# Optimization experiments

Measured on AMD Instinct MI355X. Metric: run time of the kernel, lower is better.

Reference implementation:

```python
import jax, jax.numpy as jnp
import numpy as np

D_NUM, P_NUM, LAYER, EMB = 1500, 4500, 3, 128


def _xavier(k, shape):
    lim = float(np.sqrt(6.0 / (shape[0] + shape[1])))
    return jax.random.uniform(k, shape, minval=-lim, maxval=lim, dtype=jnp.float32)


def _sym_norm(adj):
    # D^{-1/2} A D^{-1/2}, zero-degree safe (utils._create_*_adj_mat)
    deg = adj.sum(axis=1)
    dinv = jnp.where(deg > 0, jax.lax.rsqrt(jnp.maximum(deg, 1e-12)), 0.0)
    return adj * dinv[:, None] * dinv[None, :]


def _gcn(adj, emb, num):
    # LightGCN-style propagation: mean of layer-0..num embeddings (utils._gcn)
    def step(e, _):
        e = adj @ e
        return e, e
    _, layers = jax.lax.scan(step, emb, None, length=num)
    return (emb + layers.sum(axis=0)) / (num + 1)


def _neighbor_mean(mat, feats):
    # vectorized form of the per-row python loop: mean of feats over j where mat[i,j]==1, zeros if no neighbor
    m = (mat == 1.0).astype(feats.dtype)
    cnt = m.sum(axis=1, keepdims=True)
    return jnp.where(cnt > 0, (m @ feats) / jnp.maximum(cnt, 1.0), 0.0)


def _get_weight(emb, WA, BA, HA):
    return jax.nn.log_softmax(jax.nn.relu(emb @ WA + BA) @ HA, axis=0)


def setup_inputs():
    k = jax.random.split(jax.random.key(0), 24)
    N = D_NUM + P_NUM
    A = (jax.random.uniform(k[0], (5, N, N)) < 0.005).astype(jnp.float32)
    z = lambda: jnp.zeros((EMB,), jnp.float32)
    h = lambda: jnp.full((EMB, 1), 0.01, jnp.float32)
    return {
        "A": A,
        "drug_structure": jax.random.normal(k[1], (D_NUM, 160), jnp.float32),
        "protein_structure": jax.random.normal(k[2], (P_NUM, 512), jnp.float32),
        "lin_drug_w": _xavier(k[3], (160, EMB)), "lin_drug_b": z(),
        "lin_pro_w": _xavier(k[4], (512, EMB)), "lin_pro_b": z(),
        "p_weight": _xavier(k[5], (EMB, EMB)),
        "d_weight_i": _xavier(k[6], (EMB, EMB)),
        "pd_weight_p": _xavier(k[7], (EMB, EMB)),
        "pd_weight_d": _xavier(k[8], (EMB, EMB)),
        "dp_weight_p": _xavier(k[9], (EMB, EMB)),
        "WA_drug": _xavier(k[10], (EMB, EMB)), "BA_drug": z(), "HA_drug": h(),
        "WB_drug": _xavier(k[11], (EMB, EMB)), "BB_drug": z(), "HB_drug": h(),
        "WA_pro": _xavier(k[12], (EMB, EMB)), "BA_pro": z(), "HA_pro": h(),
        "WB_pro": _xavier(k[13], (EMB, EMB)), "BB_pro": z(), "HB_pro": h(),
        "WA_sim": _xavier(k[14], (EMB, EMB)), "BA_sim": z(), "HA_sim": h(),
        "layer": LAYER,
    }


def reference(A, drug_structure, protein_structure, lin_drug_w, lin_drug_b, lin_pro_w, lin_pro_b,
              p_weight, d_weight_i, pd_weight_p, pd_weight_d, dp_weight_p,
              WA_drug, BA_drug, HA_drug, WB_drug, BB_drug, HB_drug,
              WA_pro, BA_pro, HA_pro, WB_pro, BB_pro, HB_pro,
              WA_sim, BA_sim, HA_sim, layer):
    D, P = D_NUM, P_NUM
    R = A[0, :D, D:D + P]                       # drug-protein relation [D,P]
    dru_str = drug_structure @ lin_drug_w + lin_drug_b      # [D,128]
    pro_str = protein_structure @ lin_pro_w + lin_pro_b     # [P,128]

    def rel_emb(mat, feats, w):
        nei = _neighbor_mean(mat, feats)
        adj = _sym_norm((mat == 1.0).astype(feats.dtype))
        return _gcn(adj, feats @ w, layer), nei

    dru_rel_emb, dru_rel_nei = rel_emb(A[2, :D, :D], dru_str, d_weight_i)
    pro_rel_emb, pro_rel_nei = rel_emb(A[3, D:, D:], pro_str, p_weight)
    dru_sim_emb, dru_sim_nei = rel_emb(A[4, :D, :D], dru_str, d_weight_i)

    dru_tem = _neighbor_mean(R, pro_rel_nei)    # [D,128]
    # NB: torch 'dru_rel_nei + dru_sim_nei' concatenates python LISTS, and only
    # indices < D are ever read, so pro_tem effectively uses dru_rel_nei only.
    pro_tem = _neighbor_mean(R.T, dru_rel_nei)  # [P,128]

    # bipartite symmetric-normalized adjacency [[0,R],[R^T,0]]
    bip = jnp.zeros((D + P, D + P), R.dtype)
    bip = bip.at[:D, D:].set(R).at[D:, :D].set(R.T)
    adj = _sym_norm(bip)

    one_all = 0.8 * dru_str + 0.2 * dru_tem
    two_all = 0.8 * pro_str + 0.2 * pro_tem
    one_emb = dru_str @ pd_weight_d
    two_all = (two_all @ dp_weight_p) @ pd_weight_d
    two_emb = pro_str @ pd_weight_p
    dru_int = _gcn(adj, jnp.concatenate([one_emb, two_all], axis=0), layer)[:D]
    pro_int = _gcn(adj, jnp.concatenate([one_all, two_emb], axis=0), layer)[D:]

    drug_w = _get_weight(dru_int, WA_drug, BA_drug, HA_drug)
    pro_w = _get_weight(pro_int, WA_pro, BA_pro, HA_pro)
    dru_rel_w = _get_weight(dru_rel_emb, WB_drug, BB_drug, HB_drug)
    pro_rel_w = _get_weight(pro_rel_emb, WB_pro, BB_pro, HB_pro)
    dru_sim_w = _get_weight(dru_sim_emb, WA_sim, BA_sim, HA_sim)

    # faithful to source (including its asymmetric renormalization); dropout is eval-mode identity
    a_w = drug_w / (drug_w + dru_rel_w + dru_sim_w)
    b_w = dru_rel_w / (a_w + dru_rel_w + dru_sim_w)
    c_w = 1.0 - a_w - b_w
    fin_dru = a_w * dru_int + b_w * dru_rel_emb + c_w * dru_sim_emb

    pa = pro_w / (pro_w + pro_rel_w)
    pb = 1.0 - pa
    fin_pro = pa * pro_int + pb * pro_rel_emb

    y = fin_dru @ fin_pro.T                     # [D,P]
    y = (y - y.mean()) / jnp.std(y, ddof=1)     # torch.std is unbiased
    return jax.nn.sigmoid(y)
```

## Files before the change

### kernel.cpp

```cpp
#include <hip/hip_runtime.h>

constexpr int CAP = 128;
constexpr int RS_INV = 1, RS_RSQRT = 2, CS_RSQRT = 4, FINALIZE = 8;

struct BuildSeg {
    const float* M; long ldm; int rows; int cols; int col_off;
    int* idx; int* cnt;
};

__global__ void k_build_all(BuildSeg sa, BuildSeg sb, BuildSeg sc, BuildSeg sd,
                            int zb, int e0, int e1, int e2,
                            int* __restrict__ zcnt, int nz, double* __restrict__ stats)
{
    int blk = blockIdx.x;
    if (blk < zb) {
        int i = blk * 256 + threadIdx.x;
        if (i < nz) zcnt[i] = 0;
        if (blk == 0 && threadIdx.x < 2) stats[threadIdx.x] = 0.0;
        return;
    }
    BuildSeg s; int lb;
    if (blk < e0)      { s = sa; lb = blk - zb; }
    else if (blk < e1) { s = sb; lb = blk - e0; }
    else if (blk < e2) { s = sc; lb = blk - e1; }
    else               { s = sd; lb = blk - e2; }
    int row = lb * 4 + (threadIdx.x >> 6);
    if (row >= s.rows) return;
    int lane = threadIdx.x & 63;
    const float* p = s.M + (long)row * s.ldm;
    int* ri = s.idx + (long)row * CAP;
    int base = 0;
    for (int j0 = 0; j0 < s.cols; j0 += 64) {
        int j = j0 + lane;
        bool hit = (j < s.cols) && (p[j] == 1.0f);
        unsigned long long m = __ballot(hit);
        if (hit) {
            int pos = base + (int)__popcll(m & ((1ULL << lane) - 1ULL));
            if (pos < CAP) ri[pos] = j + s.col_off;
        }
        base += (int)__popcll(m);
    }
    if (lane == 0) s.cnt[row] = base < CAP ? base : CAP;
}

__global__ void k_scatter_T(int* __restrict__ idx, int* __restrict__ cnt, int topRows)
{
    int row = blockIdx.x * 4 + (threadIdx.x >> 6);
    if (row >= topRows) return;
    int lane = threadIdx.x & 63;
    int n = cnt[row];
    const int* ri = idx + (long)row * CAP;
    for (int k = lane; k < n; k += 64) {
        int j = ri[k];
        int pos = atomicAdd(&cnt[j], 1);
        if (pos < CAP) idx[(long)j * CAP + pos] = row;
    }
}

struct SpmmJob {
    const int* idx; const int* cnt; int rows; int mod;
    const float* X; float* out; float* acc; const float* init; float* fin;
    int flags;
};

__global__ __launch_bounds__(256)
void k_spmm_multi(SpmmJob ja, SpmmJob jb, int nb0)
{
    SpmmJob j; int lb;
    if ((int)blockIdx.x < nb0) { j = ja; lb = blockIdx.x; }
    else                       { j = jb; lb = blockIdx.x - nb0; }
    int c = threadIdx.x & 127;
    int row = lb * 2 + (threadIdx.x >> 7);
    if (row >= j.rows) return;
    int r_loc = row, xoff = 0;
    if (row >= j.mod) { r_loc = row - j.mod; xoff = j.mod; }
    int n = j.cnt[r_loc];
    const int* ri = j.idx + (long)r_loc * CAP;
    const bool csq = (j.flags & CS_RSQRT) != 0;
    float acc = 0.0f;
    int k = 0;
    for (; k + 4 <= n; k += 4) {
        int c0 = ri[k], c1 = ri[k + 1], c2 = ri[k + 2], c3 = ri[k + 3];
        float x0 = j.X[(long)(c0 + xoff) * 128 + c];
        float x1 = j.X[(long)(c1 + xoff) * 128 + c];
        float x2 = j.X[(long)(c2 + xoff) * 128 + c];
        float x3 = j.X[(long)(c3 + xoff) * 128 + c];
        if (csq) {
            int n0 = j.cnt[c0], n1 = j.cnt[c1], n2 = j.cnt[c2], n3 = j.cnt[c3];
            x0 *= (n0 > 0) ? rsqrtf((float)n0) : 0.0f;
            x1 *= (n1 > 0) ? rsqrtf((float)n1) : 0.0f;
            x2 *= (n2 > 0) ? rsqrtf((float)n2) : 0.0f;
            x3 *= (n3 > 0) ? rsqrtf((float)n3) : 0.0f;
        }
        acc += (x0 + x1) + (x2 + x3);
    }
    for (; k < n; ++k) {
        int cj = ri[k];
        float x = j.X[(long)(cj + xoff) * 128 + c];
        if (csq) {
            int nj = j.cnt[cj];
            x *= (nj > 0) ? rsqrtf((float)nj) : 0.0f;
        }
        acc += x;
    }
    float v;
    if (j.flags & RS_INV)        v = (n > 0) ? acc / (float)n : 0.0f;
    else if (j.flags & RS_RSQRT) v = (n > 0) ? acc * rsqrtf((float)n) : 0.0f;
    else                         v = acc;
    long o = (long)row * 128 + c;
    if (j.flags & FINALIZE) {
        j.fin[o] = (j.acc[o] + v) * 0.25f;
    } else {
        j.out[o] = v;
        if (j.acc) j.acc[o] = (j.init ? j.init[o] : j.acc[o]) + v;
    }
}

struct LinJob {
    const float* X; const float* X2; float pa, pb; int rows; int K;
    const float* W; const float* bias; float* out; float* out2;
};

__global__ __launch_bounds__(256)
void k_lin_multi(LinJob j0, LinJob j1, LinJob j2, LinJob j3,
                 int e0, int e1, int e2)
{
    __shared__ float Ws[64 * 128];
    LinJob j; int lb;
    int blk = blockIdx.x;
    if (blk < e0)      { j = j0; lb = blk; }
    else if (blk < e1) { j = j1; lb = blk - e0; }
    else if (blk < e2) { j = j2; lb = blk - e1; }
    else               { j = j3; lb = blk - e2; }
    int c = threadIdx.x & 127;
    int row = lb * 2 + (threadIdx.x >> 7);
    if (j.W == nullptr) {
        if (row < j.rows) {
            long o = (long)row * 128 + c;
            float v = j.pa * j.X[o] + j.pb * j.X2[o];
            j.out[o] = v;
            if (j.out2) j.out2[o] = v;
        }
        return;
    }
    float acc = 0.0f;
    for (int k0 = 0; k0 < j.K; k0 += 64) {
        int chunk = min(64, j.K - k0);
        for (int e = threadIdx.x; e < chunk * 128; e += 256)
            Ws[e] = j.W[(long)(k0 + (e >> 7)) * 128 + (e & 127)];
        __syncthreads();
        if (row < j.rows) {
            const float* xr = j.X + (long)row * j.K + k0;
            const float* x2r = j.X2 ? j.X2 + (long)row * j.K + k0 : nullptr;
            #pragma unroll 4
            for (int kk = 0; kk < chunk; ++kk) {
                float v = xr[kk];
                if (j.X2) v = j.pa * v + j.pb * x2r[kk];
                acc += v * Ws[kk * 128 + c];
            }
        }
        __syncthreads();
    }
    if (row < j.rows) {
        float v = acc + (j.bias ? j.bias[c] : 0.0f);
        j.out[(long)row * 128 + c] = v;
        if (j.out2) j.out2[(long)row * 128 + c] = v;
    }
}

struct AttnJob { const float* X; int rows; const float* W; const float* B;
                 const float* H; float* s; };

__global__ __launch_bounds__(256)
void k_attn_multi(AttnJob a0, AttnJob a1, AttnJob a2, AttnJob a3, AttnJob a4,
                  int e0, int e1, int e2, int e3)
{
    __shared__ float Ws[64 * 128];
    __shared__ float part[4];
    AttnJob j; int lb;
    int blk = blockIdx.x;
    if (blk < e0)      { j = a0; lb = blk; }
    else if (blk < e1) { j = a1; lb = blk - e0; }
    else if (blk < e2) { j = a2; lb = blk - e1; }
    else if (blk < e3) { j = a3; lb = blk - e2; }
    else               { j = a4; lb = blk - e3; }
    int c = threadIdx.x & 127;
    int row = lb * 2 + (threadIdx.x >> 7);
    float acc = 0.0f;
    for (int k0 = 0; k0 < 128; k0 += 64) {
        for (int e = threadIdx.x; e < 64 * 128; e += 256)
            Ws[e] = j.W[(long)(k0 + (e >> 7)) * 128 + (e & 127)];
        __syncthreads();
        if (row < j.rows) {
            const float* xr = j.X + (long)row * 128 + k0;
            #pragma unroll 4
            for (int kk = 0; kk < 64; ++kk)
                acc += xr[kk] * Ws[kk * 128 + c];
        }
        __syncthreads();
    }
    float v = 0.0f;
    if (row < j.rows) v = fmaxf(acc + j.B[c], 0.0f) * j.H[c];
    for (int o = 32; o > 0; o >>= 1) v += __shfl_down(v, o, 64);
    if ((threadIdx.x & 63) == 0) part[threadIdx.x >> 6] = v;
    __syncthreads();
    if (threadIdx.x == 0 && row < j.rows)   j.s[row] = part[0] + part[1];
    if (threadIdx.x == 128 && row < j.rows) j.s[row] = part[2] + part[3];
}

__global__ void k_logsoftmax5(float* s0, int n0, float* s1, int n1,
                              float* s2, int n2, float* s3, int n3,
                              float* s4, int n4)
{
    float* s; int n;
    switch (blockIdx.x) {
        case 0: s = s0; n = n0; break;
        case 1: s = s1; n = n1; break;
        case 2: s = s2; n = n2; break;
        case 3: s = s3; n = n3; break;
        default: s = s4; n = n4; break;
    }
    __shared__ float red[256];
    int t = threadIdx.x;
    float m = -3.4e38f;
    for (int i = t; i < n; i += 256) m = fmaxf(m, s[i]);
    red[t] = m; __syncthreads();
    for (int o = 128; o > 0; o >>= 1) {
        if (t < o) red[t] = fmaxf(red[t], red[t + o]);
        __syncthreads();
    }
    m = red[0];
    __syncthreads();
    float sum = 0.0f;
    for (int i = t; i < n; i += 256) sum += expf(s[i] - m);
    red[t] = sum; __syncthreads();
    for (int o = 128; o > 0; o >>= 1) {
        if (t < o) red[t] += red[t + o];
        __syncthreads();
    }
    float lse = m + logf(red[0]);
    for (int i = t; i < n; i += 256) s[i] -= lse;
}

__global__ void k_fin(const float* __restrict__ wd, const float* __restrict__ wdr,
                      const float* __restrict__ wds,
                      const float* __restrict__ ei, const float* __restrict__ er,
                      const float* __restrict__ es,
                      const float* __restrict__ wp, const float* __restrict__ wpr,
                      const float* __restrict__ pi, const float* __restrict__ pr,
                      float* __restrict__ fd, float* __restrict__ fp,
                      long nDel, long total)
{
    long i = (long)blockIdx.x * 256 + threadIdx.x;
    if (i >= total) return;
    if (i < nDel) {
        int r = (int)(i >> 7);
        float aL = wd[r], bL = wdr[r], cL = wds[r];
        float a = aL / (aL + bL + cL);
        float b = bL / (a + bL + cL);
        float c = 1.0f - a - b;
        fd[i] = a * ei[i] + b * er[i] + c * es[i];
    } else {
        long k = i - nDel;
        int r = (int)(k >> 7);
        float pa = wp[r] / (wp[r] + wpr[r]);
        fp[k] = pa * pi[k] + (1.0f - pa) * pr[k];
    }
}

__global__ __launch_bounds__(256)
void k_ygemm(const float* __restrict__ Af, const float* __restrict__ Bf,
             int M, int N, float* __restrict__ y, double* __restrict__ stats)
{
    __shared__ float Ast[32][68];
    __shared__ float Bst[32][68];
    int i0 = blockIdx.y * 64, j0 = blockIdx.x * 64;
    int tx = threadIdx.x & 15, ty = threadIdx.x >> 4;
    float acc[4][4] = {};
    for (int k0 = 0; k0 < 128; k0 += 32) {
        for (int e = threadIdx.x; e < 64 * 32; e += 256) {
            int r = e >> 5, kk = e & 31;
            int ia = i0 + r, jb = j0 + r;
            Ast[kk][r] = (ia < M) ? Af[(long)ia * 128 + k0 + kk] : 0.0f;
            Bst[kk][r] = (jb < N) ? Bf[(long)jb * 128 + k0 + kk] : 0.0f;
        }
        __syncthreads();
        #pragma unroll 8
        for (int kk = 0; kk < 32; ++kk) {
            float a0 = Ast[kk][ty * 4 + 0], a1 = Ast[kk][ty * 4 + 1];
            float a2 = Ast[kk][ty * 4 + 2], a3 = Ast[kk][ty * 4 + 3];
            float b0 = Bst[kk][tx * 4 + 0], b1 = Bst[kk][tx * 4 + 1];
            float b2 = Bst[kk][tx * 4 + 2], b3 = Bst[kk][tx * 4 + 3];
            acc[0][0] += a0 * b0; acc[0][1] += a0 * b1; acc[0][2] += a0 * b2; acc[0][3] += a0 * b3;
            acc[1][0] += a1 * b0; acc[1][1] += a1 * b1; acc[1][2] += a1 * b2; acc[1][3] += a1 * b3;
            acc[2][0] += a2 * b0; acc[2][1] += a2 * b1; acc[2][2] += a2 * b2; acc[2][3] += a2 * b3;
            acc[3][0] += a3 * b0; acc[3][1] += a3 * b1; acc[3][2] += a3 * b2; acc[3][3] += a3 * b3;
        }
        __syncthreads();
    }
    double s1 = 0.0, s2 = 0.0;
    #pragma unroll
    for (int q = 0; q < 4; ++q) {
        int i = i0 + ty * 4 + q;
        if (i < M) {
            #pragma unroll
            for (int p = 0; p < 4; ++p) {
                int j = j0 + tx * 4 + p;
                if (j < N) {
                    float v = acc[q][p];
                    y[(long)i * N + j] = v;
                    s1 += v; s2 += (double)v * v;
                }
            }
        }
    }
    __shared__ double r1[256];
    __shared__ double r2[256];
    r1[threadIdx.x] = s1; r2[threadIdx.x] = s2;
    __syncthreads();
    for (int o = 128; o > 0; o >>= 1) {
        if (threadIdx.x < o) {
            r1[threadIdx.x] += r1[threadIdx.x + o];
            r2[threadIdx.x] += r2[threadIdx.x + o];
        }
        __syncthreads();
    }
    if (threadIdx.x == 0) {
        atomicAdd(&stats[0], r1[0]);
        atomicAdd(&stats[1], r2[0]);
    }
}

__global__ void k_sigmoid(const float* __restrict__ y, const double* __restrict__ stats,
                          long n, float* __restrict__ out)
{
    long i = (long)blockIdx.x * 256 + threadIdx.x;
    if (i >= n) return;
    double nd = (double)n;
    double mean = stats[0] / nd;
    double var = (stats[1] - nd * mean * mean) / (nd - 1.0);
    if (var < 1e-30) var = 1e-30;
    float inv = (float)(1.0 / sqrt(var));
    float mu = (float)mean;
    out[i] = 1.0f / (1.0f + expf(-((y[i] - mu) * inv)));
}

extern "C" void kernel_launch(void* const* d_in, const int* in_sizes, int n_in,
                              void* d_out, int out_size, void* d_ws, size_t ws_size,
                              hipStream_t stream)
{
    constexpr int D = 1500, P = 4500, E = 128;
    constexpr int NB = D + P;
    constexpr int NR = D + P + D;
    constexpr long ALD = 6000;
    constexpr long ASZ = 36000000L;

    const float* A    = (const float*)d_in[0];
    const float* drug_structure    = (const float*)d_in[1];
    const float* protein_structure = (const float*)d_in[2];
    const float* lin_drug_w = (const float*)d_in[3];
    const float* lin_drug_b = (const float*)d_in[4];
    const float* lin_pro_w  = (const float*)d_in[5];
    const float* lin_pro_b  = (const float*)d_in[6];
    const float* p_weight   = (const float*)d_in[7];
    const float* d_weight_i = (const float*)d_in[8];
    const float* pd_weight_p = (const float*)d_in[9];
    const float* pd_weight_d = (const float*)d_in[10];
    const float* dp_weight_p = (const float*)d_in[11];
    const float* WA_drug = (const float*)d_in[12];
    const float* BA_drug = (const float*)d_in[13];
    const float* HA_drug = (const float*)d_in[14];
    const float* WB_drug = (const float*)d_in[15];
    const float* BB_drug = (const float*)d_in[16];
    const float* HB_drug = (const float*)d_in[17];
    const float* WA_pro = (const float*)d_in[18];
    const float* BA_pro = (const float*)d_in[19];
    const float* HA_pro = (const float*)d_in[20];
    const float* WB_pro = (const float*)d_in[21];
    const float* BB_pro = (const float*)d_in[22];
    const float* HB_pro = (const float*)d_in[23];
    const float* WA_sim = (const float*)d_in[24];
    const float* BA_sim = (const float*)d_in[25];
    const float* HA_sim = (const float*)d_in[26];

    const float* Rp  = A + 1500;
    const float* A2p = A + 2 * ASZ;
    const float* A3p = A + 3 * ASZ + 1500 * ALD + 1500;
    const float* A4p = A + 4 * ASZ;

    char* wsbase = (char*)d_ws;
    size_t off = 0;
    auto alloc = [&](size_t bytes) -> void* {
        off = (off + 255) & ~(size_t)255;
        void* p = wsbase + off;
        off += bytes;
        return p;
    };
    int*   idx_bip  = (int*)alloc((size_t)NB * CAP * 4);
    int*   cnt_bip  = (int*)alloc((size_t)NB * 4);
    int*   idx_rel  = (int*)alloc((size_t)NR * CAP * 4);
    int*   cnt_rel  = (int*)alloc((size_t)NR * 4);
    float* str_s    = (float*)alloc((size_t)NR * E * 4);
    float* nei_s    = (float*)alloc((size_t)NR * E * 4);
    float* cur_s    = (float*)alloc((size_t)NR * E * 4);
    float* nxt_s    = (float*)alloc((size_t)NR * E * 4);
    float* acc_s    = (float*)alloc((size_t)NR * E * 4);
    float* emb_s    = (float*)alloc((size_t)NR * E * 4);
    float* tem_s    = (float*)alloc((size_t)NB * E * 4);
    float* big_cur  = (float*)alloc((size_t)2 * NB * E * 4);
    float* big_nxt  = (float*)alloc((size_t)2 * NB * E * 4);
    float* big_acc  = (float*)alloc((size_t)2 * NB * E * 4);
    float* int_s    = (float*)alloc((size_t)2 * NB * E * 4);
    float* W2       = (float*)alloc((size_t)E * E * 4);
    float* w_drug = (float*)alloc(D * 4);
    float* w_drel = (float*)alloc(D * 4);
    float* w_dsim = (float*)alloc(D * 4);
    float* w_pro  = (float*)alloc(P * 4);
    float* w_prel = (float*)alloc(P * 4);
    float* fin_dru = (float*)alloc((size_t)D * E * 4);
    float* fin_pro = (float*)alloc((size_t)P * E * 4);
    float* ybuf    = (float*)alloc((size_t)D * P * 4);
    double* stats  = (double*)alloc(2 * sizeof(double));
    (void)ws_size; (void)in_sizes; (void)n_in; (void)out_size;

    float* dru_str = str_s;
    float* pro_str = str_s + (size_t)D * E;
    float* dru_rel_emb = emb_s;
    float* pro_rel_emb = emb_s + (size_t)D * E;
    float* dru_sim_emb = emb_s + (size_t)NB * E;
    float* dru_tem = tem_s;
    float* pro_tem = tem_s + (size_t)D * E;
    float* dru_int = int_s;
    float* pro_int = int_s + (size_t)(NB + D) * E;

    long nD = (long)D * E, nP = (long)P * E;

    SpmmJob JZ = {};
    LinJob  LZ = {};

    {
        BuildSeg sR  = { Rp,  ALD, D, P, D,  idx_bip, cnt_bip };
        BuildSeg sA2 = { A2p, ALD, D, D, 0,  idx_rel, cnt_rel };
        BuildSeg sA3 = { A3p, ALD, P, P, D,  idx_rel + (size_t)D * CAP,  cnt_rel + D };
        BuildSeg sA4 = { A4p, ALD, D, D, NB, idx_rel + (size_t)NB * CAP, cnt_rel + NB };
        int zb = (P + 255) / 256;
        int e0 = zb + (D + 3) / 4;
        int e1 = e0 + (D + 3) / 4;
        int e2 = e1 + (P + 3) / 4;
        int total = e2 + (D + 3) / 4;
        k_build_all<<<total, 256, 0, stream>>>(sR, sA2, sA3, sA4, zb, e0, e1, e2,
                                               cnt_bip + D, P, stats);
    }
    k_scatter_T<<<(D + 3) / 4, 256, 0, stream>>>(idx_bip, cnt_bip, D);

    {
        LinJob jd = { drug_structure, nullptr, 0, 0, D, 160, lin_drug_w, lin_drug_b,
                      dru_str, str_s + (size_t)NB * E };
        LinJob jp = { protein_structure, nullptr, 0, 0, P, 512, lin_pro_w, lin_pro_b,
                      pro_str, nullptr };
        LinJob jw = { dp_weight_p, nullptr, 0, 0, E, E, pd_weight_d, nullptr, W2, nullptr };
        int e0 = (D + 1) / 2, e1 = e0 + (P + 1) / 2, e2 = e1 + (E + 1) / 2;
        k_lin_multi<<<e2, 256, 0, stream>>>(jd, jp, jw, LZ, e0, e1, e2);
    }
    {
        SpmmJob jn = { idx_rel, cnt_rel, NR, NR, str_s, nei_s, nullptr, nullptr, nullptr, RS_INV };
        k_spmm_multi<<<(NR + 1) / 2, 256, 0, stream>>>(jn, JZ, (NR + 1) / 2);
    }
    {
        LinJob jd = { dru_str, nullptr, 0, 0, D, E, d_weight_i, nullptr,
                      cur_s, cur_s + (size_t)NB * E };
        LinJob jp = { pro_str, nullptr, 0, 0, P, E, p_weight, nullptr,
                      cur_s + (size_t)D * E, nullptr };
        int e0 = (D + 1) / 2, e1 = e0 + (P + 1) / 2;
        k_lin_multi<<<e1, 256, 0, stream>>>(jd, jp, LZ, LZ, e0, e1, e1);
    }
    {
        SpmmJob j1 = { idx_rel, cnt_rel, NR, NR, cur_s, nxt_s, acc_s, cur_s, nullptr,
                       RS_RSQRT | CS_RSQRT };
        SpmmJob j2 = { idx_bip, cnt_bip, NB, NB, nei_s, tem_s, nullptr, nullptr, nullptr,
                       RS_INV };
        int nb0 = (NR + 1) / 2, nb1 = (NB + 1) / 2;
        k_spmm_multi<<<nb0 + nb1, 256, 0, stream>>>(j1, j2, nb0);
    }
    {
        LinJob j0 = { dru_str, nullptr, 0, 0, D, E, pd_weight_d, nullptr, big_cur, nullptr };
        LinJob j1 = { pro_str, pro_tem, 0.8f, 0.2f, P, E, W2, nullptr, big_cur + nD, nullptr };
        LinJob j2 = { dru_str, dru_tem, 0.8f, 0.2f, D, E, nullptr, nullptr,
                      big_cur + (size_t)NB * E, nullptr };
        LinJob j3 = { pro_str, nullptr, 0, 0, P, E, pd_weight_p, nullptr,
                      big_cur + (size_t)(NB + D) * E, nullptr };
        int e0 = (D + 1) / 2, e1 = e0 + (P + 1) / 2, e2 = e1 + (D + 1) / 2;
        int tt = e2 + (P + 1) / 2;
        k_lin_multi<<<tt, 256, 0, stream>>>(j0, j1, j2, j3, e0, e1, e2);
    }
    {
        SpmmJob j1 = { idx_rel, cnt_rel, NR, NR, nxt_s, cur_s, acc_s, nullptr, nullptr,
                       RS_RSQRT | CS_RSQRT };
        SpmmJob j2 = { idx_bip, cnt_bip, 2 * NB, NB, big_cur, big_nxt, big_acc, big_cur,
                       nullptr, RS_RSQRT | CS_RSQRT };
        int nb0 = (NR + 1) / 2;
        k_spmm_multi<<<nb0 + NB, 256, 0, stream>>>(j1, j2, nb0);
    }
    {
        SpmmJob j1 = { idx_rel, cnt_rel, NR, NR, cur_s, nullptr, acc_s, nullptr, emb_s,
                       RS_RSQRT | CS_RSQRT | FINALIZE };
        SpmmJob j2 = { idx_bip, cnt_bip, 2 * NB, NB, big_nxt, big_cur, big_acc, nullptr,
                       nullptr, RS_RSQRT | CS_RSQRT };
        int nb0 = (NR + 1) / 2;
        k_spmm_multi<<<nb0 + NB, 256, 0, stream>>>(j1, j2, nb0);
    }
    {
        SpmmJob j2 = { idx_bip, cnt_bip, 2 * NB, NB, big_cur, nullptr, big_acc, nullptr,
                       int_s, RS_RSQRT | CS_RSQRT | FINALIZE };
        k_spmm_multi<<<NB, 256, 0, stream>>>(j2, JZ, NB);
    }
    {
        AttnJob a0 = { dru_int,     D, WA_drug, BA_drug, HA_drug, w_drug };
        AttnJob a1 = { pro_int,     P, WA_pro,  BA_pro,  HA_pro,  w_pro  };
        AttnJob a2 = { dru_rel_emb, D, WB_drug, BB_drug, HB_drug, w_drel };
        AttnJob a3 = { pro_rel_emb, P, WB_pro,  BB_pro,  HB_pro,  w_prel };
        AttnJob a4 = { dru_sim_emb, D, WA_sim,  BA_sim,  HA_sim,  w_dsim };
        int e0 = (D + 1) / 2, e1 = e0 + (P + 1) / 2, e2 = e1 + (D + 1) / 2;
        int e3 = e2 + (P + 1) / 2, tt = e3 + (D + 1) / 2;
        k_attn_multi<<<tt, 256, 0, stream>>>(a0, a1, a2, a3, a4, e0, e1, e2, e3);
    }
    k_logsoftmax5<<<5, 256, 0, stream>>>(w_drug, D, w_pro, P, w_drel, D, w_prel, P, w_dsim, D);

    {
        long total = nD + nP;
        k_fin<<<(int)((total + 255) / 256), 256, 0, stream>>>(
            w_drug, w_drel, w_dsim, dru_int, dru_rel_emb, dru_sim_emb,
            w_pro, w_prel, pro_int, pro_rel_emb,
            fin_dru, fin_pro, nD, total);
    }
    dim3 yg((P + 63) / 64, (D + 63) / 64);
    k_ygemm<<<yg, 256, 0, stream>>>(fin_dru, fin_pro, D, P, ybuf, stats);
    long ny = (long)D * P;
    k_sigmoid<<<(int)((ny + 255) / 256), 256, 0, stream>>>(ybuf, stats, ny, (float*)d_out);
}
```

Before: 1.373 ms.

## Fuse all stages into one cooperative persistent kernel with grid syncs

Replaces the chain of separate launches (build, scatter, linear, spmm, attention, softmax, fin, gemm, sigmoid) with a single cooperative kernel of 512 persistent blocks that loops over tiles and uses grid-wide syncs between dependent phases. Independent work is placed together in the same phase, such as the relation spmm with linear jobs and the attention on relation embeddings with a bipartite spmm layer. The goal is to remove per-launch overhead and idle gaps between small kernels. In exchange it adds grid-sync cost, caps parallelism at the fixed grid size, hardcodes job tile boundaries for these problem sizes, and the sigmoid now uses float4 with no tail handling.

```diff
diff --git a/kernel.cpp b/kernel.cpp
--- a/kernel.cpp
+++ b/kernel.cpp
@@ -1,29 +1,54 @@
 #include <hip/hip_runtime.h>
+#include <hip/hip_cooperative_groups.h>
+
+namespace cg = cooperative_groups;
 
 constexpr int CAP = 128;
 constexpr int RS_INV = 1, RS_RSQRT = 2, CS_RSQRT = 4, FINALIZE = 8;
-
-struct BuildSeg {
-    const float* M; long ldm; int rows; int cols; int col_off;
-    int* idx; int* cnt;
+constexpr int GRID = 512;
+
+struct BuildSeg { const float* M; long ldm; int rows; int cols; int col_off;
+                  int* idx; int* cnt; };
+struct LinJob  { const float* X; const float* X2; float pa, pb; int rows; int K;
+                 const float* W; const float* bias; float* out; float* out2; };
+struct SpmmJob { const int* idx; const int* cnt; int rows; int mod;
+                 const float* X; float* out; float* acc; const float* init;
+                 float* fin; int flags; };
+struct AttnJob { const float* X; int rows; const float* W; const float* B;
+                 const float* H; float* s; };
+
+struct MegaArgs {
+    BuildSeg bs[4]; int bsEnd[4];
+    int* zcnt; int nz; double* stats;
+    int* idx_bip; int* cnt_bip; int scatterUnits; int scatterTop;
+    LinJob pj[3]; int pjEnd[3];
+    SpmmJob relNei;
+    LinJob rj[2]; int rjEnd[2];
+    SpmmJob relL1, bipNei;
+    LinJob bj[4]; int bjEnd[4];
+    SpmmJob relL2;
+    SpmmJob bipL1, relL3;
+    SpmmJob bipL2;
+    AttnJob atR[3]; int atREnd[3];
+    SpmmJob bipL3;
+    float* smv[5]; int smn[5];
+    AttnJob atI[2]; int atIEnd[2];
+    const float *wd, *wdr, *wds, *ei, *er, *es, *wp, *wpr, *pi, *pr;
+    float *fd, *fp; long nDel, totFin;
+    const float *Af, *Bf; int M, N; float* y;
+    float* outp; long ny;
 };
 
-__global__ void k_build_all(BuildSeg sa, BuildSeg sb, BuildSeg sc, BuildSeg sd,
-                            int zb, int e0, int e1, int e2,
-                            int* __restrict__ zcnt, int nz, double* __restrict__ stats)
-{
-    int blk = blockIdx.x;
-    if (blk < zb) {
-        int i = blk * 256 + threadIdx.x;
-        if (i < nz) zcnt[i] = 0;
-        if (blk == 0 && threadIdx.x < 2) stats[threadIdx.x] = 0.0;
-        return;
-    }
-    BuildSeg s; int lb;
-    if (blk < e0)      { s = sa; lb = blk - zb; }
-    else if (blk < e1) { s = sb; lb = blk - e0; }
-    else if (blk < e2) { s = sc; lb = blk - e1; }
-    else               { s = sd; lb = blk - e2; }
+union SharedU {
+    float Ws[64 * 128];
+    struct { float Ast[32][68]; float Bst[32][68];
+             double r1[256]; double r2[256]; } yg;
+    float red[256];
+};
+
+
+__device__ __forceinline__ void build_unit(const BuildSeg& s, int lb)
+{
     int row = lb * 4 + (threadIdx.x >> 6);
     if (row >= s.rows) return;
     int lane = threadIdx.x & 63;
@@ -31,21 +56,21 @@
     int* ri = s.idx + (long)row * CAP;
     int base = 0;
     for (int j0 = 0; j0 < s.cols; j0 += 64) {
-        int j = j0 + lane;
-        bool hit = (j < s.cols) && (p[j] == 1.0f);
+        int jj = j0 + lane;
+        bool hit = (jj < s.cols) && (p[jj] == 1.0f);
         unsigned long long m = __ballot(hit);
         if (hit) {
             int pos = base + (int)__popcll(m & ((1ULL << lane) - 1ULL));
-            if (pos < CAP) ri[pos] = j + s.col_off;
+            if (pos < CAP) ri[pos] = jj + s.col_off;
         }
         base += (int)__popcll(m);
     }
     if (lane == 0) s.cnt[row] = base < CAP ? base : CAP;
 }
 
-__global__ void k_scatter_T(int* __restrict__ idx, int* __restrict__ cnt, int topRows)
-{
-    int row = blockIdx.x * 4 + (threadIdx.x >> 6);
+__device__ __forceinline__ void scatter_unit(int* idx, int* cnt, int topRows, int lb)
+{
+    int row = lb * 4 + (threadIdx.x >> 6);
     if (row >= topRows) return;
     int lane = threadIdx.x & 63;
     int n = cnt[row];
@@ -57,18 +82,8 @@
     }
 }
 
-struct SpmmJob {
-    const int* idx; const int* cnt; int rows; int mod;
-    const float* X; float* out; float* acc; const float* init; float* fin;
-    int flags;
-};
-
-__global__ __launch_bounds__(256)
-void k_spmm_multi(SpmmJob ja, SpmmJob jb, int nb0)
-{
-    SpmmJob j; int lb;
-    if ((int)blockIdx.x < nb0) { j = ja; lb = blockIdx.x; }
-    else                       { j = jb; lb = blockIdx.x - nb0; }
+__device__ __forceinline__ void spmm_tile(const SpmmJob& j, int lb)
+{
     int c = threadIdx.x & 127;
     int row = lb * 2 + (threadIdx.x >> 7);
     if (row >= j.rows) return;
@@ -116,22 +131,23 @@
     }
 }
 
-struct LinJob {
-    const float* X; const float* X2; float pa, pb; int rows; int K;
-    const float* W; const float* bias; float* out; float* out2;
-};
-
-__global__ __launch_bounds__(256)
-void k_lin_multi(LinJob j0, LinJob j1, LinJob j2, LinJob j3,
-                 int e0, int e1, int e2)
-{
-    __shared__ float Ws[64 * 128];
-    LinJob j; int lb;
-    int blk = blockIdx.x;
-    if (blk < e0)      { j = j0; lb = blk; }
-    else if (blk < e1) { j = j1; lb = blk - e0; }
-    else if (blk < e2) { j = j2; lb = blk - e1; }
-    else               { j = j3; lb = blk - e2; }
+__device__ void run_spmm1(const SpmmJob& a)
+{
+    int ta = (a.rows + 1) / 2;
+    for (int t = blockIdx.x; t < ta; t += gridDim.x) spmm_tile(a, t);
+}
+
+__device__ void run_spmm2(const SpmmJob& a, const SpmmJob& b)
+{
+    int ta = (a.rows + 1) / 2, tb = (b.rows + 1) / 2;
+    for (int t = blockIdx.x; t < ta + tb; t += gridDim.x) {
+        if (t < ta) spmm_tile(a, t);
+        else        spmm_tile(b, t - ta);
+    }
+}
+
+__device__ void lin_tile(const LinJob& j, int lb, float* Ws)
+{
     int c = threadIdx.x & 127;
     int row = lb * 2 + (threadIdx.x >> 7);
     if (j.W == nullptr) {
@@ -168,22 +184,20 @@
     }
 }
 
-struct AttnJob { const float* X; int rows; const float* W; const float* B;
-                 const float* H; float* s; };
-
-__global__ __launch_bounds__(256)
-void k_attn_multi(AttnJob a0, AttnJob a1, AttnJob a2, AttnJob a3, AttnJob a4,
-                  int e0, int e1, int e2, int e3)
-{
-    __shared__ float Ws[64 * 128];
+__device__ void run_lin(const LinJob* jobs, const int* ends, int nj, float* Ws)
+{
+    int tot = ends[nj - 1];
+    for (int t = blockIdx.x; t < tot; t += gridDim.x) {
+        int ji = 0;
+        while (t >= ends[ji]) ++ji;
+        int lb = t - (ji ? ends[ji - 1] : 0);
+        lin_tile(jobs[ji], lb, Ws);
+    }
+}
+
+__device__ void attn_tile(const AttnJob& j, int lb, float* Ws)
+{
     __shared__ float part[4];
-    AttnJob j; int lb;
-    int blk = blockIdx.x;
-    if (blk < e0)      { j = a0; lb = blk; }
-    else if (blk < e1) { j = a1; lb = blk - e0; }
-    else if (blk < e2) { j = a2; lb = blk - e1; }
-    else if (blk < e3) { j = a3; lb = blk - e2; }
-    else               { j = a4; lb = blk - e3; }
     int c = threadIdx.x & 127;
     int row = lb * 2 + (threadIdx.x >> 7);
     float acc = 0.0f;
@@ -208,19 +222,19 @@
     if (threadIdx.x == 128 && row < j.rows) j.s[row] = part[2] + part[3];
 }
 
-__global__ void k_logsoftmax5(float* s0, int n0, float* s1, int n1,
-                              float* s2, int n2, float* s3, int n3,
-                              float* s4, int n4)
-{
-    float* s; int n;
-    switch (blockIdx.x) {
-        case 0: s = s0; n = n0; break;
-        case 1: s = s1; n = n1; break;
-        case 2: s = s2; n = n2; break;
-        case 3: s = s3; n = n3; break;
-        default: s = s4; n = n4; break;
-    }
-    __shared__ float red[256];
+__device__ void run_attn(const AttnJob* jobs, const int* ends, int nj, float* Ws)
+{
+    int tot = ends[nj - 1];
+    for (int t = blockIdx.x; t < tot; t += gridDim.x) {
+        int ji = 0;
+        while (t >= ends[ji]) ++ji;
+        int lb = t - (ji ? ends[ji - 1] : 0);
+        attn_tile(jobs[ji], lb, Ws);
+    }
+}
+
+__device__ void softmax_vec(float* s, int n, float* red)
+{
     int t = threadIdx.x;
     float m = -3.4e38f;
     for (int i = t; i < n; i += 256) m = fmaxf(m, s[i]);
@@ -242,55 +256,46 @@
     for (int i = t; i < n; i += 256) s[i] -= lse;
 }
 
-__global__ void k_fin(const float* __restrict__ wd, const float* __restrict__ wdr,
-                      const float* __restrict__ wds,
-                      const float* __restrict__ ei, const float* __restrict__ er,
-                      const float* __restrict__ es,
-                      const float* __restrict__ wp, const float* __restrict__ wpr,
-                      const float* __restrict__ pi, const float* __restrict__ pr,
-                      float* __restrict__ fd, float* __restrict__ fp,
-                      long nDel, long total)
-{
-    long i = (long)blockIdx.x * 256 + threadIdx.x;
-    if (i >= total) return;
-    if (i < nDel) {
-        int r = (int)(i >> 7);
-        float aL = wd[r], bL = wdr[r], cL = wds[r];
-        float a = aL / (aL + bL + cL);
-        float b = bL / (a + bL + cL);
-        float c = 1.0f - a - b;
-        fd[i] = a * ei[i] + b * er[i] + c * es[i];
-    } else {
-        long k = i - nDel;
-        int r = (int)(k >> 7);
-        float pa = wp[r] / (wp[r] + wpr[r]);
-        fp[k] = pa * pi[k] + (1.0f - pa) * pr[k];
-    }
-}
-
-__global__ __launch_bounds__(256)
-void k_ygemm(const float* __restrict__ Af, const float* __restrict__ Bf,
-             int M, int N, float* __restrict__ y, double* __restrict__ stats)
-{
-    __shared__ float Ast[32][68];
-    __shared__ float Bst[32][68];
-    int i0 = blockIdx.y * 64, j0 = blockIdx.x * 64;
+__device__ void run_fin(const MegaArgs& a)
+{
+    long g = (long)blockIdx.x * 256 + threadIdx.x;
+    long gs = (long)gridDim.x * 256;
+    for (long i = g; i < a.totFin; i += gs) {
+        if (i < a.nDel) {
+            int r = (int)(i >> 7);
+            float aL = a.wd[r], bL = a.wdr[r], cL = a.wds[r];
+            float x = aL / (aL + bL + cL);
+            float y = bL / (x + bL + cL);
+            float z = 1.0f - x - y;
+            a.fd[i] = x * a.ei[i] + y * a.er[i] + z * a.es[i];
+        } else {
+            long k = i - a.nDel;
+            int r = (int)(k >> 7);
+            float pa = a.wp[r] / (a.wp[r] + a.wpr[r]);
+            a.fp[k] = pa * a.pi[k] + (1.0f - pa) * a.pr[k];
+        }
+    }
+}
+
+__device__ void ygemm_tile(const MegaArgs& a, int bx, int by, SharedU& sh)
+{
+    int i0 = by * 64, j0 = bx * 64;
     int tx = threadIdx.x & 15, ty = threadIdx.x >> 4;
     float acc[4][4] = {};
     for (int k0 = 0; k0 < 128; k0 += 32) {
         for (int e = threadIdx.x; e < 64 * 32; e += 256) {
             int r = e >> 5, kk = e & 31;
             int ia = i0 + r, jb = j0 + r;
-            Ast[kk][r] = (ia < M) ? Af[(long)ia * 128 + k0 + kk] : 0.0f;
-            Bst[kk][r] = (jb < N) ? Bf[(long)jb * 128 + k0 + kk] : 0.0f;
+            sh.yg.Ast[kk][r] = (ia < a.M) ? a.Af[(long)ia * 128 + k0 + kk] : 0.0f;
+            sh.yg.Bst[kk][r] = (jb < a.N) ? a.Bf[(long)jb * 128 + k0 + kk] : 0.0f;
         }
         __syncthreads();
         #pragma unroll 8
         for (int kk = 0; kk < 32; ++kk) {
-            float a0 = Ast[kk][ty * 4 + 0], a1 = Ast[kk][ty * 4 + 1];
-            float a2 = Ast[kk][ty * 4 + 2], a3 = Ast[kk][ty * 4 + 3];
-            float b0 = Bst[kk][tx * 4 + 0], b1 = Bst[kk][tx * 4 + 1];
-            float b2 = Bst[kk][tx * 4 + 2], b3 = Bst[kk][tx * 4 + 3];
+            float a0 = sh.yg.Ast[kk][ty * 4 + 0], a1 = sh.yg.Ast[kk][ty * 4 + 1];
+            float a2 = sh.yg.Ast[kk][ty * 4 + 2], a3 = sh.yg.Ast[kk][ty * 4 + 3];
+            float b0 = sh.yg.Bst[kk][tx * 4 + 0], b1 = sh.yg.Bst[kk][tx * 4 + 1];
+            float b2 = sh.yg.Bst[kk][tx * 4 + 2], b3 = sh.yg.Bst[kk][tx * 4 + 3];
             acc[0][0] += a0 * b0; acc[0][1] += a0 * b1; acc[0][2] += a0 * b2; acc[0][3] += a0 * b3;
             acc[1][0] += a1 * b0; acc[1][1] += a1 * b1; acc[1][2] += a1 * b2; acc[1][3] += a1 * b3;
             acc[2][0] += a2 * b0; acc[2][1] += a2 * b1; acc[2][2] += a2 * b2; acc[2][3] += a2 * b3;
@@ -302,47 +307,113 @@
     #pragma unroll
     for (int q = 0; q < 4; ++q) {
         int i = i0 + ty * 4 + q;
-        if (i < M) {
+        if (i < a.M) {
             #pragma unroll
             for (int p = 0; p < 4; ++p) {
                 int j = j0 + tx * 4 + p;
-                if (j < N) {
+                if (j < a.N) {
                     float v = acc[q][p];
-                    y[(long)i * N + j] = v;
+                    a.y[(long)i * a.N + j] = v;
                     s1 += v; s2 += (double)v * v;
                 }
             }
         }
     }
-    __shared__ double r1[256];
-    __shared__ double r2[256];
-    r1[threadIdx.x] = s1; r2[threadIdx.x] = s2;
+    sh.yg.r1[threadIdx.x] = s1; sh.yg.r2[threadIdx.x] = s2;
     __syncthreads();
     for (int o = 128; o > 0; o >>= 1) {
         if (threadIdx.x < o) {
-            r1[threadIdx.x] += r1[threadIdx.x + o];
-            r2[threadIdx.x] += r2[threadIdx.x + o];
+            sh.yg.r1[threadIdx.x] += sh.yg.r1[threadIdx.x + o];
+            sh.yg.r2[threadIdx.x] += sh.yg.r2[threadIdx.x + o];
         }
         __syncthreads();
     }
     if (threadIdx.x == 0) {
-        atomicAdd(&stats[0], r1[0]);
-        atomicAdd(&stats[1], r2[0]);
-    }
-}
-
-__global__ void k_sigmoid(const float* __restrict__ y, const double* __restrict__ stats,
-                          long n, float* __restrict__ out)
-{
-    long i = (long)blockIdx.x * 256 + threadIdx.x;
-    if (i >= n) return;
-    double nd = (double)n;
-    double mean = stats[0] / nd;
-    double var = (stats[1] - nd * mean * mean) / (nd - 1.0);
+        atomicAdd(&a.stats[0], sh.yg.r1[0]);
+        atomicAdd(&a.stats[1], sh.yg.r2[0]);
+    }
+}
+
+__device__ void run_ygemm(const MegaArgs& a, SharedU& sh)
+{
+    int tilesX = (a.N + 63) / 64, tilesY = (a.M + 63) / 64;
+    int tot = tilesX * tilesY;
+    for (int t = blockIdx.x; t < tot; t += gridDim.x)
+        ygemm_tile(a, t % tilesX, t / tilesX, sh);
+}
+
+__device__ void run_sigmoid(const MegaArgs& a)
+{
+    double nd = (double)a.ny;
+    double mean = a.stats[0] / nd;
+    double var = (a.stats[1] - nd * mean * mean) / (nd - 1.0);
     if (var < 1e-30) var = 1e-30;
     float inv = (float)(1.0 / sqrt(var));
     float mu = (float)mean;
-    out[i] = 1.0f / (1.0f + expf(-((y[i] - mu) * inv)));
+    long n4 = a.ny >> 2;
+    const float4* y4 = (const float4*)a.y;
+    float4* o4 = (float4*)a.outp;
+    long g = (long)blockIdx.x * 256 + threadIdx.x;
+    long gs = (long)gridDim.x * 256;
+    for (long i = g; i < n4; i += gs) {
+        float4 v = y4[i];
+        v.x = 1.0f / (1.0f + expf(-((v.x - mu) * inv)));
+        v.y = 1.0f / (1.0f + expf(-((v.y - mu) * inv)));
+        v.z = 1.0f / (1.0f + expf(-((v.z - mu) * inv)));
+        v.w = 1.0f / (1.0f + expf(-((v.w - mu) * inv)));
+        o4[i] = v;
+    }
+}
+
+__global__ __launch_bounds__(256, 2)
+void k_mega(MegaArgs a)
+{
+    cg::grid_group grid = cg::this_grid();
+    __shared__ SharedU sh;
+
+    {
+        long g = (long)blockIdx.x * 256 + threadIdx.x;
+        long gs = (long)gridDim.x * 256;
+        for (long i = g; i < a.nz; i += gs) a.zcnt[i] = 0;
+        if (blockIdx.x == 0 && threadIdx.x < 2) a.stats[threadIdx.x] = 0.0;
+        for (int u = blockIdx.x; u < a.bsEnd[3]; u += gridDim.x) {
+            int si = 0;
+            while (u >= a.bsEnd[si]) ++si;
+            int lb = u - (si ? a.bsEnd[si - 1] : 0);
+            build_unit(a.bs[si], lb);
+        }
+        run_lin(a.pj, a.pjEnd, 3, sh.Ws);
+    }
+    grid.sync();
+    {
+        for (int u = blockIdx.x; u < a.scatterUnits; u += gridDim.x)
+            scatter_unit(a.idx_bip, a.cnt_bip, a.scatterTop, u);
+        run_spmm1(a.relNei);
+        run_lin(a.rj, a.rjEnd, 2, sh.Ws);
+    }
+    grid.sync();
+    run_spmm2(a.relL1, a.bipNei);
+    grid.sync();
+    run_lin(a.bj, a.bjEnd, 4, sh.Ws);
+    run_spmm1(a.relL2);
+    grid.sync();
+    run_spmm2(a.bipL1, a.relL3);
+    grid.sync();
+    run_spmm1(a.bipL2);
+    run_attn(a.atR, a.atREnd, 3, sh.Ws);
+    grid.sync();
+    run_spmm1(a.bipL3);
+    if (blockIdx.x < 3) softmax_vec(a.smv[blockIdx.x], a.smn[blockIdx.x], sh.red);
+    grid.sync();
+    run_attn(a.atI, a.atIEnd, 2, sh.Ws);
+    grid.sync();
+    if (blockIdx.x < 2) softmax_vec(a.smv[3 + blockIdx.x], a.smn[3 + blockIdx.x], sh.red);
+    grid.sync();
+    run_fin(a);
+    grid.sync();
+    run_ygemm(a, sh);
+    grid.sync();
+    run_sigmoid(a);
 }
 
 extern "C" void kernel_launch(void* const* d_in, const int* in_sizes, int n_in,
@@ -435,106 +506,80 @@
 
     long nD = (long)D * E, nP = (long)P * E;
 
-    SpmmJob JZ = {};
-    LinJob  LZ = {};
-
-    {
-        BuildSeg sR  = { Rp,  ALD, D, P, D,  idx_bip, cnt_bip };
-        BuildSeg sA2 = { A2p, ALD, D, D, 0,  idx_rel, cnt_rel };
-        BuildSeg sA3 = { A3p, ALD, P, P, D,  idx_rel + (size_t)D * CAP,  cnt_rel + D };
-        BuildSeg sA4 = { A4p, ALD, D, D, NB, idx_rel + (size_t)NB * CAP, cnt_rel + NB };
-        int zb = (P + 255) / 256;
-        int e0 = zb + (D + 3) / 4;
-        int e1 = e0 + (D + 3) / 4;
-        int e2 = e1 + (P + 3) / 4;
-        int total = e2 + (D + 3) / 4;
-        k_build_all<<<total, 256, 0, stream>>>(sR, sA2, sA3, sA4, zb, e0, e1, e2,
-                                               cnt_bip + D, P, stats);
-    }
-    k_scatter_T<<<(D + 3) / 4, 256, 0, stream>>>(idx_bip, cnt_bip, D);
-
-    {
-        LinJob jd = { drug_structure, nullptr, 0, 0, D, 160, lin_drug_w, lin_drug_b,
-                      dru_str, str_s + (size_t)NB * E };
-        LinJob jp = { protein_structure, nullptr, 0, 0, P, 512, lin_pro_w, lin_pro_b,
-                      pro_str, nullptr };
-        LinJob jw = { dp_weight_p, nullptr, 0, 0, E, E, pd_weight_d, nullptr, W2, nullptr };
-        int e0 = (D + 1) / 2, e1 = e0 + (P + 1) / 2, e2 = e1 + (E + 1) / 2;
-        k_lin_multi<<<e2, 256, 0, stream>>>(jd, jp, jw, LZ, e0, e1, e2);
-    }
-    {
-        SpmmJob jn = { idx_rel, cnt_rel, NR, NR, str_s, nei_s, nullptr, nullptr, nullptr, RS_INV };
-        k_spmm_multi<<<(NR + 1) / 2, 256, 0, stream>>>(jn, JZ, (NR + 1) / 2);
-    }
-    {
-        LinJob jd = { dru_str, nullptr, 0, 0, D, E, d_weight_i, nullptr,
-                      cur_s, cur_s + (size_t)NB * E };
-        LinJob jp = { pro_str, nullptr, 0, 0, P, E, p_weight, nullptr,
-                      cur_s + (size_t)D * E, nullptr };
-        int e0 = (D + 1) / 2, e1 = e0 + (P + 1) / 2;
-        k_lin_multi<<<e1, 256, 0, stream>>>(jd, jp, LZ, LZ, e0, e1, e1);
-    }
-    {
-        SpmmJob j1 = { idx_rel, cnt_rel, NR, NR, cur_s, nxt_s, acc_s, cur_s, nullptr,
-                       RS_RSQRT | CS_RSQRT };
-        SpmmJob j2 = { idx_bip, cnt_bip, NB, NB, nei_s, tem_s, nullptr, nullptr, nullptr,
-                       RS_INV };
-        int nb0 = (NR + 1) / 2, nb1 = (NB + 1) / 2;
-        k_spmm_multi<<<nb0 + nb1, 256, 0, stream>>>(j1, j2, nb0);
-    }
-    {
-        LinJob j0 = { dru_str, nullptr, 0, 0, D, E, pd_weight_d, nullptr, big_cur, nullptr };
-        LinJob j1 = { pro_str, pro_tem, 0.8f, 0.2f, P, E, W2, nullptr, big_cur + nD, nullptr };
-        LinJob j2 = { dru_str, dru_tem, 0.8f, 0.2f, D, E, nullptr, nullptr,
-                      big_cur + (size_t)NB * E, nullptr };
-        LinJob j3 = { pro_str, nullptr, 0, 0, P, E, pd_weight_p, nullptr,
-                      big_cur + (size_t)(NB + D) * E, nullptr };
-        int e0 = (D + 1) / 2, e1 = e0 + (P + 1) / 2, e2 = e1 + (D + 1) / 2;
-        int tt = e2 + (P + 1) / 2;
-        k_lin_multi<<<tt, 256, 0, stream>>>(j0, j1, j2, j3, e0, e1, e2);
-    }
-    {
-        SpmmJob j1 = { idx_rel, cnt_rel, NR, NR, nxt_s, cur_s, acc_s, nullptr, nullptr,
-                       RS_RSQRT | CS_RSQRT };
-        SpmmJob j2 = { idx_bip, cnt_bip, 2 * NB, NB, big_cur, big_nxt, big_acc, big_cur,
-                       nullptr, RS_RSQRT | CS_RSQRT };
-        int nb0 = (NR + 1) / 2;
-        k_spmm_multi<<<nb0 + NB, 256, 0, stream>>>(j1, j2, nb0);
-    }
-    {
-        SpmmJob j1 = { idx_rel, cnt_rel, NR, NR, cur_s, nullptr, acc_s, nullptr, emb_s,
-                       RS_RSQRT | CS_RSQRT | FINALIZE };
-        SpmmJob j2 = { idx_bip, cnt_bip, 2 * NB, NB, big_nxt, big_cur, big_acc, nullptr,
-                       nullptr, RS_RSQRT | CS_RSQRT };
-        int nb0 = (NR + 1) / 2;
-        k_spmm_multi<<<nb0 + NB, 256, 0, stream>>>(j1, j2, nb0);
-    }
-    {
-        SpmmJob j2 = { idx_bip, cnt_bip, 2 * NB, NB, big_cur, nullptr, big_acc, nullptr,
-                       int_s, RS_RSQRT | CS_RSQRT | FINALIZE };
-        k_spmm_multi<<<NB, 256, 0, stream>>>(j2, JZ, NB);
-    }
-    {
-        AttnJob a0 = { dru_int,     D, WA_drug, BA_drug, HA_drug, w_drug };
-        AttnJob a1 = { pro_int,     P, WA_pro,  BA_pro,  HA_pro,  w_pro  };
-        AttnJob a2 = { dru_rel_emb, D, WB_drug, BB_drug, HB_drug, w_drel };
-        AttnJob a3 = { pro_rel_emb, P, WB_pro,  BB_pro,  HB_pro,  w_prel };
-        AttnJob a4 = { dru_sim_emb, D, WA_sim,  BA_sim,  HA_sim,  w_dsim };
-        int e0 = (D + 1) / 2, e1 = e0 + (P + 1) / 2, e2 = e1 + (D + 1) / 2;
-        int e3 = e2 + (P + 1) / 2, tt = e3 + (D + 1) / 2;
-        k_attn_multi<<<tt, 256, 0, stream>>>(a0, a1, a2, a3, a4, e0, e1, e2, e3);
-    }
-    k_logsoftmax5<<<5, 256, 0, stream>>>(w_drug, D, w_pro, P, w_drel, D, w_prel, P, w_dsim, D);
-
-    {
-        long total = nD + nP;
-        k_fin<<<(int)((total + 255) / 256), 256, 0, stream>>>(
-            w_drug, w_drel, w_dsim, dru_int, dru_rel_emb, dru_sim_emb,
-            w_pro, w_prel, pro_int, pro_rel_emb,
-            fin_dru, fin_pro, nD, total);
-    }
-    dim3 yg((P + 63) / 64, (D + 63) / 64);
-    k_ygemm<<<yg, 256, 0, stream>>>(fin_dru, fin_pro, D, P, ybuf, stats);
-    long ny = (long)D * P;
-    k_sigmoid<<<(int)((ny + 255) / 256), 256, 0, stream>>>(ybuf, stats, ny, (float*)d_out);
-}
+    MegaArgs a;
+    a.bs[0] = { Rp,  ALD, D, P, D,  idx_bip, cnt_bip };
+    a.bs[1] = { A2p, ALD, D, D, 0,  idx_rel, cnt_rel };
+    a.bs[2] = { A3p, ALD, P, P, D,  idx_rel + (size_t)D * CAP,  cnt_rel + D };
+    a.bs[3] = { A4p, ALD, D, D, NB, idx_rel + (size_t)NB * CAP, cnt_rel + NB };
+    a.bsEnd[0] = 375; a.bsEnd[1] = 750; a.bsEnd[2] = 1875; a.bsEnd[3] = 2250;
+    a.zcnt = cnt_bip + D; a.nz = P; a.stats = stats;
+    a.idx_bip = idx_bip; a.cnt_bip = cnt_bip;
+    a.scatterUnits = (D + 3) / 4; a.scatterTop = D;
+
+    a.pj[0] = { drug_structure, nullptr, 0, 0, D, 160, lin_drug_w, lin_drug_b,
+                dru_str, str_s + (size_t)NB * E };
+    a.pj[1] = { protein_structure, nullptr, 0, 0, P, 512, lin_pro_w, lin_pro_b,
+                pro_str, nullptr };
+    a.pj[2] = { dp_weight_p, nullptr, 0, 0, E, E, pd_weight_d, nullptr, W2, nullptr };
+    a.pjEnd[0] = 750; a.pjEnd[1] = 3000; a.pjEnd[2] = 3064;
+
+    a.relNei = { idx_rel, cnt_rel, NR, NR, str_s, nei_s, nullptr, nullptr, nullptr, RS_INV };
+
+    a.rj[0] = { dru_str, nullptr, 0, 0, D, E, d_weight_i, nullptr,
+                cur_s, cur_s + (size_t)NB * E };
+    a.rj[1] = { pro_str, nullptr, 0, 0, P, E, p_weight, nullptr,
+                cur_s + (size_t)D * E, nullptr };
+    a.rjEnd[0] = 750; a.rjEnd[1] = 3000;
+
+    a.relL1 = { idx_rel, cnt_rel, NR, NR, cur_s, nxt_s, acc_s, cur_s, nullptr,
+                RS_RSQRT | CS_RSQRT };
+    a.bipNei = { idx_bip, cnt_bip, NB, NB, nei_s, tem_s, nullptr, nullptr, nullptr,
+                 RS_INV };
+
+    a.bj[0] = { dru_str, nullptr, 0, 0, D, E, pd_weight_d, nullptr, big_cur, nullptr };
+    a.bj[1] = { pro_str, pro_tem, 0.8f, 0.2f, P, E, W2, nullptr, big_cur + nD, nullptr };
+    a.bj[2] = { dru_str, dru_tem, 0.8f, 0.2f, D, E, nullptr, nullptr,
+                big_cur + (size_t)NB * E, nullptr };
+    a.bj[3] = { pro_str, nullptr, 0, 0, P, E, pd_weight_p, nullptr,
+                big_cur + (size_t)(NB + D) * E, nullptr };
+    a.bjEnd[0] = 750; a.bjEnd[1] = 3000; a.bjEnd[2] = 3750; a.bjEnd[3] = 6000;
+
+    a.relL2 = { idx_rel, cnt_rel, NR, NR, nxt_s, cur_s, acc_s, nullptr, nullptr,
+                RS_RSQRT | CS_RSQRT };
+    a.bipL1 = { idx_bip, cnt_bip, 2 * NB, NB, big_cur, big_nxt, big_acc, big_cur,
+                nullptr, RS_RSQRT | CS_RSQRT };
+    a.relL3 = { idx_rel, cnt_rel, NR, NR, cur_s, nullptr, acc_s, nullptr, emb_s,
+                RS_RSQRT | CS_RSQRT | FINALIZE };
+    a.bipL2 = { idx_bip, cnt_bip, 2 * NB, NB, big_nxt, big_cur, big_acc, nullptr,
+                nullptr, RS_RSQRT | CS_RSQRT };
+
+    a.atR[0] = { dru_rel_emb, D, WB_drug, BB_drug, HB_drug, w_drel };
+    a.atR[1] = { pro_rel_emb, P, WB_pro,  BB_pro,  HB_pro,  w_prel };
+    a.atR[2] = { dru_sim_emb, D, WA_sim,  BA_sim,  HA_sim,  w_dsim };
+    a.atREnd[0] = 750; a.atREnd[1] = 3000; a.atREnd[2] = 3750;
+
+    a.bipL3 = { idx_bip, cnt_bip, 2 * NB, NB, big_cur, nullptr, big_acc, nullptr,
+                int_s, RS_RSQRT | CS_RSQRT | FINALIZE };
+
+    a.smv[0] = w_drel; a.smn[0] = D;
+    a.smv[1] = w_prel; a.smn[1] = P;
+    a.smv[2] = w_dsim; a.smn[2] = D;
+    a.smv[3] = w_drug; a.smn[3] = D;
+    a.smv[4] = w_pro;  a.smn[4] = P;
+
+    a.atI[0] = { dru_int, D, WA_drug, BA_drug, HA_drug, w_drug };
+    a.atI[1] = { pro_int, P, WA_pro,  BA_pro,  HA_pro,  w_pro  };
+    a.atIEnd[0] = 750; a.atIEnd[1] = 3000;
+
+    a.wd = w_drug; a.wdr = w_drel; a.wds = w_dsim;
+    a.ei = dru_int; a.er = dru_rel_emb; a.es = dru_sim_emb;
+    a.wp = w_pro; a.wpr = w_prel; a.pi = pro_int; a.pr = pro_rel_emb;
+    a.fd = fin_dru; a.fp = fin_pro; a.nDel = nD; a.totFin = nD + nP;
+
+    a.Af = fin_dru; a.Bf = fin_pro; a.M = D; a.N = P; a.y = ybuf;
+    a.outp = (float*)d_out; a.ny = (long)D * P;
+
+    void* params[] = { &a };
+    hipLaunchCooperativeKernel((void*)k_mega, dim3(GRID), dim3(256),
+                               params, 0, stream);
+}
```

Measured after the change: 2.608 ms. 90.0% more time.
